# Kernel tuning notes

Measured on AMD Instinct MI355X. Metric: run time of the kernel, lower is better.

The kernel has to match this reference:

```python
import jax, jax.numpy as jnp
import numpy as np
from jax.scipy.special import i0

B, P = 2, 524288
N = (512, 512)            # uniform frequency grid
M = 4                     # window cutoff m (2M taps per dim)
SIGMA = 2.0
NGRID = tuple(2 * (int(SIGMA * Ni) // 2) for Ni in N)  # oversampled grid (1024, 1024)
BETA = tuple(float(np.pi * (2.0 - 1.0 / (ng / Ni))) for ng, Ni in zip(NGRID, N))


def _phi_hat_1d(Ni, ni, b):
    # Fourier coefficients of the Kaiser-Bessel window, k = -Ni/2 .. Ni/2-1
    k = jnp.arange(-Ni // 2, Ni // 2, dtype=jnp.float32)
    arg = jnp.sqrt(b * b - (2.0 * jnp.pi * k / ni) ** 2)
    return i0(M * arg) / ni


def _window_ft():
    # separable d-dim Fourier coefficient grid, shape [N1, N2] (== window.ft)
    c1 = _phi_hat_1d(N[0], NGRID[0], BETA[0])
    c2 = _phi_hat_1d(N[1], NGRID[1], BETA[1])
    return c1[:, None] * c2[None, :]


def _phi(t, ni, b):
    # Kaiser-Bessel window in time domain, support |t| <= M/ni
    u2 = M * M - (ni * t) ** 2
    u = jnp.sqrt(jnp.maximum(u2, 1e-12))
    return jnp.where(u2 > 0, jnp.sinh(b * u) / (jnp.pi * u), 0.0)


def setup_inputs() -> dict:
    key = jax.random.key(0)
    k1, k2 = jax.random.split(key)
    x = jax.random.uniform(k1, (B, P, 2), jnp.float32, -0.5, 0.5)  # points on torus
    f_hat = jax.random.normal(k2, (B, N[0], N[1], 2), jnp.float32)  # complex as [re,im]
    return {"x": x, "f_hat": f_hat}


def _nfft_forward(x, f_hat):
    # f(x_j) ~= sum_k f_hat[k] exp(-2 pi i <k, x_j>) via window-deconvolved oversampled FFT + local gather
    fh = (f_hat[..., 0] + 1j * f_hat[..., 1]).astype(jnp.complex64)  # [B, N1, N2]
    ft = _window_ft().astype(jnp.float32)
    gh = fh / ft                                                    # deconvolve
    p1 = (NGRID[0] - N[0]) // 2
    p2 = (NGRID[1] - N[1]) // 2
    gh = jnp.pad(gh, ((0, 0), (p1, p1), (p2, p2)))                  # centered zero-pad to n
    g = jnp.fft.fftn(jnp.fft.ifftshift(gh, axes=(-2, -1)), axes=(-2, -1))
    g = g / (NGRID[0] * NGRID[1])                                   # g_l = (1/n) sum_k gh_k e^{-2pi i kl/n}

    offs = jnp.arange(-M + 1, M + 1)                                # [2M]
    ws, idxs = [], []
    for d in range(2):
        nd = NGRID[d]
        xd = x[..., d]                                              # [B, P]
        l0 = jnp.floor(xd * nd).astype(jnp.int32)
        l = l0[..., None] + offs                                    # [B, P, 2M]
        t = xd[..., None] - l.astype(jnp.float32) / nd
        ws.append(_phi(t, nd, BETA[d]))
        idxs.append(jnp.mod(l, nd))

    g_flat = g.reshape(B, NGRID[0] * NGRID[1])
    acc = jnp.zeros((B, P), jnp.complex64)
    for i in range(2 * M):                                          # fixed 2m x 2m taps
        for j in range(2 * M):
            flat = idxs[0][..., i] * NGRID[1] + idxs[1][..., j]     # [B, P]
            gv = jnp.take_along_axis(g_flat, flat, axis=1)
            acc = acc + (ws[0][..., i] * ws[1][..., j]) * gv
    return jnp.stack([acc.real, acc.imag], axis=-1)                 # [B, P, 2]


def reference(x, f_hat):
    return _nfft_forward(x, f_hat)
```

## Files before the change

### kernel.cpp

```cpp
#include <hip/hip_runtime.h>

constexpr int   NGRID = 1024;
constexpr int   BATCH = 2;
constexpr int   NPTS  = 524288;
constexpr int   BINS  = 2048;
constexpr int   CAP   = 768;
constexpr float BETA  = 4.71238898038469f;
constexpr float PI_F  = 3.14159265358979f;

#define PIDX(i) ((i) + ((i) >> 4))

constexpr size_t G_BYTES  = (size_t)BATCH * NGRID * NGRID * sizeof(float2);
constexpr size_t GCNT_OFF = G_BYTES;
constexpr size_t PERM_OFF = G_BYTES + 8192;

__device__ __forceinline__ float i0f_large(float x) {
    float t = 3.75f / x;
    float p =  0.00392377f;
    p = p * t + -0.01647633f;
    p = p * t +  0.02635537f;
    p = p * t + -0.02057706f;
    p = p * t +  0.00916281f;
    p = p * t + -0.00157565f;
    p = p * t +  0.00225319f;
    p = p * t +  0.01328592f;
    p = p * t +  0.39894228f;
    return __expf(x) * rsqrtf(x) * p;
}

__device__ __forceinline__ int tile_of(float2 xv, int b) {
    int c1 = ((int)floorf(xv.x * 1024.0f)) & 1023;
    int c2 = ((int)floorf(xv.y * 1024.0f)) & 1023;
    return (b << 10) + ((c1 >> 5) << 5) + (c2 >> 5);
}

__device__ __forceinline__ float2 cmul(float2 a, float2 w) {
    return make_float2(a.x * w.x - a.y * w.y, a.x * w.y + a.y * w.x);
}

__device__ __forceinline__ int digitrev4_10(int f) {
    unsigned r = __brev((unsigned)f) >> 22;
    return (int)(((r & 0x2AAu) >> 1) | ((r & 0x155u) << 1));
}

__device__ __forceinline__ void build_tw4(float2* T, int tid, int nthreads) {
    int off = 0, q = 256, sig = 1;
    #pragma unroll
    for (int st = 0; st < 5; ++st) {
        for (int m = tid; m < 3 * q; m += nthreads) {
            int sec = 0, j = m;
            if (j >= q) { sec++; j -= q; }
            if (j >= q) { sec++; j -= q; }
            float ang = (-2.0f * PI_F / 1024.0f) * (float)((sec + 1) * j * sig);
            float sw, cw;
            __sincosf(ang, &sw, &cw);
            T[off + m] = make_float2(cw, sw);
        }
        off += 3 * q; q >>= 2; sig <<= 2;
    }
}

__device__ __forceinline__ void bfly4(float2* s, const float2* T,
                                      int bt, int q, int off) {
    int j    = bt & (q - 1);
    int base = ((bt - j) << 2) + j;
    int p0 = PIDX(base), p1 = PIDX(base + q);
    int p2 = PIDX(base + 2 * q), p3 = PIDX(base + 3 * q);
    float2 a0 = s[p0], a1 = s[p1], a2 = s[p2], a3 = s[p3];
    float2 t0 = make_float2(a0.x + a2.x, a0.y + a2.y);
    float2 t1 = make_float2(a0.x - a2.x, a0.y - a2.y);
    float2 t2 = make_float2(a1.x + a3.x, a1.y + a3.y);
    float2 t3 = make_float2(a1.x - a3.x, a1.y - a3.y);
    float2 b0 = make_float2(t0.x + t2.x, t0.y + t2.y);
    float2 b2 = make_float2(t0.x - t2.x, t0.y - t2.y);
    float2 b1 = make_float2(t1.x + t3.y, t1.y - t3.x);
    float2 b3 = make_float2(t1.x - t3.y, t1.y + t3.x);
    s[p0] = b0;
    s[p1] = cmul(b1, T[off + j]);
    s[p2] = cmul(b2, T[off + q + j]);
    s[p3] = cmul(b3, T[off + 2 * q + j]);
}

__global__ __launch_bounds__(256) void rows_and_bin(const float2* __restrict__ fh,
                                                    float2* __restrict__ g,
                                                    const float2* __restrict__ x,
                                                    int* __restrict__ gcnt,
                                                    float4* __restrict__ perm) {
    __shared__ __align__(16) char smem[16880];
    int tid = threadIdx.x;

    if (blockIdx.x < 1024) {
        float2* s = (float2*)smem;
        float2* T = (float2*)smem + 1087;
        int blk = blockIdx.x & 511;
        int b   = blockIdx.x >> 9;
        int row = (blk < 256) ? blk : blk + 512;
        int a1  = (row + 256) & 1023;

        build_tw4(T, tid, 256);

        float k1 = (float)(a1 - 256);
        float w1 = (2.0f * PI_F / 1024.0f) * k1;
        float c1 = i0f_large(4.0f * sqrtf(BETA * BETA - w1 * w1));

        const float2* fr = fh + ((long)b << 18) + ((long)a1 << 9);

        float w2a = (2.0f * PI_F / 1024.0f) * (float)tid;
        float c2a = i0f_large(4.0f * sqrtf(BETA * BETA - w2a * w2a));
        float w2b = (2.0f * PI_F / 1024.0f) * (float)(tid - 256);
        float c2b = i0f_large(4.0f * sqrtf(BETA * BETA - w2b * w2b));

        float2 va = fr[tid + 256];
        float2 vb = fr[tid];
        float ia = 1.0f / (c1 * c2a);
        float ib = 1.0f / (c1 * c2b);
        float2 A = make_float2(va.x * ia, va.y * ia);
        float2 B = make_float2(vb.x * ib, vb.y * ib);

        __syncthreads();

        s[PIDX(tid)]       = make_float2(A.x + B.x, A.y + B.y);
        s[PIDX(tid + 256)] = cmul(make_float2(A.x - B.y, A.y + B.x), T[tid]);
        s[PIDX(tid + 512)] = cmul(make_float2(A.x - B.x, A.y - B.y), T[256 + tid]);
        s[PIDX(tid + 768)] = cmul(make_float2(A.x + B.y, A.y - B.x), T[512 + tid]);

        int off = 768, q = 64;
        #pragma unroll
        for (int st = 0; st < 4; ++st) {
            __syncthreads();
            bfly4(s, T, tid, q, off);
            off += 3 * q; q >>= 2;
        }
        __syncthreads();

        float2* base = g + ((long)b << 20) + ((long)row << 10);
        #pragma unroll
        for (int i = 0; i < 4; ++i) {
            int idx = tid + (i << 8);
            base[idx] = s[PIDX(digitrev4_10(idx))];
        }
    } else {
        int* h = (int*)smem;
        int bblk = blockIdx.x - 1024;
        for (int i = tid; i < BINS; i += 256) h[i] = 0;
        __syncthreads();

        int base = bblk * 4096;
        int    tile[16];
        float2 pv[16];
        #pragma unroll
        for (int i = 0; i < 16; ++i) {
            int gid = base + tid + i * 256;
            pv[i]   = x[gid];
            tile[i] = tile_of(pv[i], gid >> 19);
            atomicAdd(&h[tile[i]], 1);
        }
        __syncthreads();

        #pragma unroll
        for (int j = 0; j < 8; ++j) {
            int bi = tid + j * 256;
            int c  = h[bi];
            h[bi]  = c ? atomicAdd(&gcnt[bi], c) : 0;
        }
        __syncthreads();

        #pragma unroll
        for (int i = 0; i < 16; ++i) {
            int gid = base + tid + i * 256;
            int pos = atomicAdd(&h[tile[i]], 1);
            perm[tile[i] * CAP + pos] =
                make_float4(pv[i].x, pv[i].y, __int_as_float(gid), 0.0f);
        }
    }
}

__global__ __launch_bounds__(256) void fft_cols(float2* __restrict__ g) {
    constexpr int STR = 1092;
    __shared__ float2 s[4 * STR];
    __shared__ float2 T[1023];
    int b  = blockIdx.y;
    int C0 = blockIdx.x * 4;
    int t  = threadIdx.x;
    int c  = t & 3, L = t >> 2;
    float2* gb = g + ((long)b << 20);

    build_tw4(T, t, 256);

    float2 E[16];
    #pragma unroll
    for (int m = 0; m < 4; ++m) {
        int r = L + 64 * m;
        E[m] = gb[((long)r << 10) + C0 + c];
    }
    #pragma unroll
    for (int m = 12; m < 16; ++m) {
        int r = L + 64 * m;
        E[m] = gb[((long)r << 10) + C0 + c];
    }
    __syncthreads();

    #pragma unroll
    for (int m = 0; m < 4; ++m) {
        float2 A = E[m], B = E[m + 12];
        int j = L + 64 * m;
        E[m]      = make_float2(A.x + B.x, A.y + B.y);
        E[m + 4]  = cmul(make_float2(A.x - B.y, A.y + B.x), T[j]);
        E[m + 8]  = cmul(make_float2(A.x - B.x, A.y - B.y), T[256 + j]);
        E[m + 12] = cmul(make_float2(A.x + B.y, A.y - B.x), T[512 + j]);
    }

    {
        float2 u1 = T[768 + L], u2 = T[768 + 64 + L], u3 = T[768 + 128 + L];
        #pragma unroll
        for (int a = 0; a < 4; ++a) {
            float2 a0 = E[4*a], a1 = E[4*a+1], a2 = E[4*a+2], a3 = E[4*a+3];
            float2 t0 = make_float2(a0.x + a2.x, a0.y + a2.y);
            float2 t1 = make_float2(a0.x - a2.x, a0.y - a2.y);
            float2 t2 = make_float2(a1.x + a3.x, a1.y + a3.y);
            float2 t3 = make_float2(a1.x - a3.x, a1.y - a3.y);
            E[4*a]   = make_float2(t0.x + t2.x, t0.y + t2.y);
            E[4*a+1] = cmul(make_float2(t1.x + t3.y, t1.y - t3.x), u1);
            E[4*a+2] = cmul(make_float2(t0.x - t2.x, t0.y - t2.y), u2);
            E[4*a+3] = cmul(make_float2(t1.x - t3.y, t1.y + t3.x), u3);
        }
    }

    float2* sf = s + c * STR;
    #pragma unroll
    for (int m = 0; m < 16; ++m) sf[PIDX(L + 64 * m)] = E[m];

    int off = 960, q = 16;
    #pragma unroll
    for (int st = 0; st < 3; ++st) {
        __syncthreads();
        #pragma unroll
        for (int rr = 0; rr < 4; ++rr)
            bfly4(sf, T, L + rr * 64, q, off);
        off += 3 * q; q >>= 2;
    }
    __syncthreads();

    #pragma unroll
    for (int i = 0; i < 16; ++i) {
        int r = L + i * 64;
        gb[((long)r << 10) + C0 + c] = sf[PIDX(digitrev4_10(r))];
    }
}

__global__ __launch_bounds__(256) void gather_binned(const float2* __restrict__ g,
                                                     const int* __restrict__ gcnt,
                                                     const float4* __restrict__ perm,
                                                     float2* __restrict__ out) {
    __shared__ float2 patch[37 * 37];
    int tb = blockIdx.x;
    int b  = tb >> 10;
    int tt = tb & 1023;
    int tR = tt >> 5, tC = tt & 31;
    int R0 = (tR << 5) - 2, C0 = (tC << 5) - 2;
    const float2* gb = g + ((long)b << 20);

    for (int p = threadIdx.x; p < 37 * 37; p += 256) {
        int pr = p / 37, pc = p - pr * 37;
        int gr = (R0 + pr) & 1023, gc = (C0 + pc) & 1023;
        patch[p] = gb[(gr << 10) + gc];
    }
    __syncthreads();

    int cnt = gcnt[tb];
    if (cnt > CAP) cnt = CAP;
    int off0 = tb * CAP;
    for (int i = (int)threadIdx.x; i < cnt; i += 256) {
        float4 rec = perm[off0 + i];
        int gid = __float_as_int(rec.z);

        float w1[6], w2[6];
        int rr0, cc0;
        {
            float xs = rec.x * 1024.0f;
            float fl = floorf(xs);
            float fr = xs - fl;
            rr0 = (((int)fl) & 1023) - (tR << 5);
            #pragma unroll
            for (int k = 0; k < 6; ++k) {
                float tv = fr - (float)(k - 2);
                float u2 = 16.0f - tv * tv;
                float ir = rsqrtf(u2);
                float z  = BETA * u2 * ir;
                w1[k] = __expf(z) * 0.159154943f * ir;
            }
        }
        {
            float xs = rec.y * 1024.0f;
            float fl = floorf(xs);
            float fr = xs - fl;
            cc0 = (((int)fl) & 1023) - (tC << 5);
            #pragma unroll
            for (int k = 0; k < 6; ++k) {
                float tv = fr - (float)(k - 2);
                float u2 = 16.0f - tv * tv;
                float ir = rsqrtf(u2);
                float z  = BETA * u2 * ir;
                w2[k] = __expf(z) * 0.159154943f * ir;
            }
        }

        float ar = 0.0f, ai = 0.0f;
        #pragma unroll
        for (int ii = 0; ii < 6; ++ii) {
            int pbase = (rr0 + ii) * 37 + cc0;
            float wi = w1[ii];
            #pragma unroll
            for (int jj = 0; jj < 6; ++jj) {
                float2 gv = patch[pbase + jj];
                float w = wi * w2[jj];
                ar = fmaf(w, gv.x, ar);
                ai = fmaf(w, gv.y, ai);
            }
        }
        out[gid] = make_float2(ar, ai);
    }
}

extern "C" void kernel_launch(void* const* d_in, const int* in_sizes, int n_in,
                              void* d_out, int out_size, void* d_ws, size_t ws_size,
                              hipStream_t stream) {
    const float2* x  = (const float2*)d_in[0];
    const float2* fh = (const float2*)d_in[1];
    char* ws = (char*)d_ws;
    float2* g    = (float2*)ws;
    int*    gcnt = (int*)(ws + GCNT_OFF);
    float4* perm = (float4*)(ws + PERM_OFF);

    hipMemsetAsync(gcnt, 0, BINS * sizeof(int), stream);

    rows_and_bin<<<dim3(1280), dim3(256), 0, stream>>>(fh, g, x, gcnt, perm);
    fft_cols    <<<dim3(256, BATCH), dim3(256), 0, stream>>>(g);

    gather_binned<<<dim3(BINS), dim3(256), 0, stream>>>(g, gcnt, perm, (float2*)d_out);
}
```

Measured before the change: 118.6 us.

## Fuse row FFT, binning, column FFT and gather into one persistent kernel

Replaces the three kernel launches with a single persistent kernel of 512 blocks. Each block processes several row-FFT, binning, column-FFT and gather work units, and software grid barriers built on atomic counters separate the phases. Twiddle tables are built once per block instead of once per launch, and launch gaps between phases go away. The cost is a spin-wait barrier that requires all 512 blocks to be co-resident, which risks deadlock if occupancy is too low. The gather phase also gets fewer blocks in flight, which may hurt latency hiding.

Result: slower. 266.9 us (+125.0%).

```diff
diff --git a/kernel.cpp b/kernel.cpp
--- a/kernel.cpp
+++ b/kernel.cpp
@@ -1,18 +1,22 @@
 #include <hip/hip_runtime.h>
 
-constexpr int   NGRID = 1024;
 constexpr int   BATCH = 2;
 constexpr int   NPTS  = 524288;
 constexpr int   BINS  = 2048;
 constexpr int   CAP   = 768;
+constexpr int   NBLK  = 512;
 constexpr float BETA  = 4.71238898038469f;
 constexpr float PI_F  = 3.14159265358979f;
 
 #define PIDX(i) ((i) + ((i) >> 4))
 
-constexpr size_t G_BYTES  = (size_t)BATCH * NGRID * NGRID * sizeof(float2);
+constexpr size_t G_BYTES  = (size_t)BATCH * 1024 * 1024 * sizeof(float2);
 constexpr size_t GCNT_OFF = G_BYTES;
-constexpr size_t PERM_OFF = G_BYTES + 8192;
+constexpr size_t BAR_OFF  = G_BYTES + 8192;
+constexpr size_t PERM_OFF = G_BYTES + 8192 + 64;
+
+constexpr int SMEM_BYTES = 43128;
+constexpr int T_F2_OFF   = 4368;
 
 __device__ __forceinline__ float i0f_large(float x) {
     float t = 3.75f / x;
@@ -81,111 +85,111 @@
     s[p3] = cmul(b3, T[off + 2 * q + j]);
 }
 
-__global__ __launch_bounds__(256) void rows_and_bin(const float2* __restrict__ fh,
-                                                    float2* __restrict__ g,
-                                                    const float2* __restrict__ x,
-                                                    int* __restrict__ gcnt,
-                                                    float4* __restrict__ perm) {
-    __shared__ __align__(16) char smem[16880];
-    int tid = threadIdx.x;
-
-    if (blockIdx.x < 1024) {
-        float2* s = (float2*)smem;
-        float2* T = (float2*)smem + 1087;
-        int blk = blockIdx.x & 511;
-        int b   = blockIdx.x >> 9;
-        int row = (blk < 256) ? blk : blk + 512;
-        int a1  = (row + 256) & 1023;
-
-        build_tw4(T, tid, 256);
-
-        float k1 = (float)(a1 - 256);
-        float w1 = (2.0f * PI_F / 1024.0f) * k1;
-        float c1 = i0f_large(4.0f * sqrtf(BETA * BETA - w1 * w1));
-
-        const float2* fr = fh + ((long)b << 18) + ((long)a1 << 9);
-
-        float w2a = (2.0f * PI_F / 1024.0f) * (float)tid;
-        float c2a = i0f_large(4.0f * sqrtf(BETA * BETA - w2a * w2a));
-        float w2b = (2.0f * PI_F / 1024.0f) * (float)(tid - 256);
-        float c2b = i0f_large(4.0f * sqrtf(BETA * BETA - w2b * w2b));
-
-        float2 va = fr[tid + 256];
-        float2 vb = fr[tid];
-        float ia = 1.0f / (c1 * c2a);
-        float ib = 1.0f / (c1 * c2b);
-        float2 A = make_float2(va.x * ia, va.y * ia);
-        float2 B = make_float2(vb.x * ib, vb.y * ib);
-
+__device__ __forceinline__ void grid_barrier(int* ctr) {
+    __syncthreads();
+    if (threadIdx.x == 0) {
+        __threadfence();
+        atomicAdd(ctr, 1);
+        while (atomicAdd(ctr, 0) < NBLK) __builtin_amdgcn_s_sleep(1);
+        __threadfence();
+    }
+    __syncthreads();
+}
+
+__device__ __forceinline__ void row_unit(int u, const float2* __restrict__ fh,
+                                         float2* __restrict__ g,
+                                         float2* s, const float2* T, int tid) {
+    int blk = u & 511;
+    int b   = u >> 9;
+    int row = (blk < 256) ? blk : blk + 512;
+    int a1  = (row + 256) & 1023;
+
+    float k1 = (float)(a1 - 256);
+    float w1 = (2.0f * PI_F / 1024.0f) * k1;
+    float c1 = i0f_large(4.0f * sqrtf(BETA * BETA - w1 * w1));
+
+    const float2* fr = fh + ((long)b << 18) + ((long)a1 << 9);
+
+    float w2a = (2.0f * PI_F / 1024.0f) * (float)tid;
+    float c2a = i0f_large(4.0f * sqrtf(BETA * BETA - w2a * w2a));
+    float w2b = (2.0f * PI_F / 1024.0f) * (float)(tid - 256);
+    float c2b = i0f_large(4.0f * sqrtf(BETA * BETA - w2b * w2b));
+
+    float2 va = fr[tid + 256];
+    float2 vb = fr[tid];
+    float ia = 1.0f / (c1 * c2a);
+    float ib = 1.0f / (c1 * c2b);
+    float2 A = make_float2(va.x * ia, va.y * ia);
+    float2 B = make_float2(vb.x * ib, vb.y * ib);
+
+    __syncthreads();
+
+    s[PIDX(tid)]       = make_float2(A.x + B.x, A.y + B.y);
+    s[PIDX(tid + 256)] = cmul(make_float2(A.x - B.y, A.y + B.x), T[tid]);
+    s[PIDX(tid + 512)] = cmul(make_float2(A.x - B.x, A.y - B.y), T[256 + tid]);
+    s[PIDX(tid + 768)] = cmul(make_float2(A.x + B.y, A.y - B.x), T[512 + tid]);
+
+    int off = 768, q = 64;
+    #pragma unroll
+    for (int st = 0; st < 4; ++st) {
         __syncthreads();
-
-        s[PIDX(tid)]       = make_float2(A.x + B.x, A.y + B.y);
-        s[PIDX(tid + 256)] = cmul(make_float2(A.x - B.y, A.y + B.x), T[tid]);
-        s[PIDX(tid + 512)] = cmul(make_float2(A.x - B.x, A.y - B.y), T[256 + tid]);
-        s[PIDX(tid + 768)] = cmul(make_float2(A.x + B.y, A.y - B.x), T[512 + tid]);
-
-        int off = 768, q = 64;
-        #pragma unroll
-        for (int st = 0; st < 4; ++st) {
-            __syncthreads();
-            bfly4(s, T, tid, q, off);
-            off += 3 * q; q >>= 2;
-        }
-        __syncthreads();
-
-        float2* base = g + ((long)b << 20) + ((long)row << 10);
-        #pragma unroll
-        for (int i = 0; i < 4; ++i) {
-            int idx = tid + (i << 8);
-            base[idx] = s[PIDX(digitrev4_10(idx))];
-        }
-    } else {
-        int* h = (int*)smem;
-        int bblk = blockIdx.x - 1024;
-        for (int i = tid; i < BINS; i += 256) h[i] = 0;
-        __syncthreads();
-
-        int base = bblk * 4096;
-        int    tile[16];
-        float2 pv[16];
-        #pragma unroll
-        for (int i = 0; i < 16; ++i) {
-            int gid = base + tid + i * 256;
-            pv[i]   = x[gid];
-            tile[i] = tile_of(pv[i], gid >> 19);
-            atomicAdd(&h[tile[i]], 1);
-        }
-        __syncthreads();
-
-        #pragma unroll
-        for (int j = 0; j < 8; ++j) {
-            int bi = tid + j * 256;
-            int c  = h[bi];
-            h[bi]  = c ? atomicAdd(&gcnt[bi], c) : 0;
-        }
-        __syncthreads();
-
-        #pragma unroll
-        for (int i = 0; i < 16; ++i) {
-            int gid = base + tid + i * 256;
-            int pos = atomicAdd(&h[tile[i]], 1);
-            perm[tile[i] * CAP + pos] =
-                make_float4(pv[i].x, pv[i].y, __int_as_float(gid), 0.0f);
-        }
-    }
-}
-
-__global__ __launch_bounds__(256) void fft_cols(float2* __restrict__ g) {
+        bfly4(s, T, tid, q, off);
+        off += 3 * q; q >>= 2;
+    }
+    __syncthreads();
+
+    float2* base = g + ((long)b << 20) + ((long)row << 10);
+    #pragma unroll
+    for (int i = 0; i < 4; ++i) {
+        int idx = tid + (i << 8);
+        base[idx] = s[PIDX(digitrev4_10(idx))];
+    }
+}
+
+__device__ __forceinline__ void bin_unit(int u, const float2* __restrict__ x,
+                                         int* __restrict__ gcnt,
+                                         float4* __restrict__ perm,
+                                         int* h, int tid) {
+    __syncthreads();
+    for (int i = tid; i < BINS; i += 256) h[i] = 0;
+    __syncthreads();
+
+    int base = u * 2048;
+    int    tile[8];
+    float2 pv[8];
+    #pragma unroll
+    for (int i = 0; i < 8; ++i) {
+        int gid = base + tid + i * 256;
+        pv[i]   = x[gid];
+        tile[i] = tile_of(pv[i], gid >> 19);
+        atomicAdd(&h[tile[i]], 1);
+    }
+    __syncthreads();
+
+    #pragma unroll
+    for (int j = 0; j < 8; ++j) {
+        int bi = tid + j * 256;
+        int c  = h[bi];
+        h[bi]  = c ? atomicAdd(&gcnt[bi], c) : 0;
+    }
+    __syncthreads();
+
+    #pragma unroll
+    for (int i = 0; i < 8; ++i) {
+        int gid = base + tid + i * 256;
+        int pos = atomicAdd(&h[tile[i]], 1);
+        perm[tile[i] * CAP + pos] =
+            make_float4(pv[i].x, pv[i].y, __int_as_float(gid), 0.0f);
+    }
+}
+
+__device__ __forceinline__ void cols_unit(int u, float2* __restrict__ g,
+                                          float2* s, const float2* T, int t) {
     constexpr int STR = 1092;
-    __shared__ float2 s[4 * STR];
-    __shared__ float2 T[1023];
-    int b  = blockIdx.y;
-    int C0 = blockIdx.x * 4;
-    int t  = threadIdx.x;
+    int b  = u >> 8;
+    int C0 = (u & 255) * 4;
     int c  = t & 3, L = t >> 2;
     float2* gb = g + ((long)b << 20);
-
-    build_tw4(T, t, 256);
 
     float2 E[16];
     #pragma unroll
@@ -198,7 +202,6 @@
         int r = L + 64 * m;
         E[m] = gb[((long)r << 10) + C0 + c];
     }
-    __syncthreads();
 
     #pragma unroll
     for (int m = 0; m < 4; ++m) {
@@ -248,19 +251,19 @@
     }
 }
 
-__global__ __launch_bounds__(256) void gather_binned(const float2* __restrict__ g,
-                                                     const int* __restrict__ gcnt,
-                                                     const float4* __restrict__ perm,
-                                                     float2* __restrict__ out) {
-    __shared__ float2 patch[37 * 37];
-    int tb = blockIdx.x;
+__device__ __forceinline__ void gather_unit(int tb, const float2* __restrict__ g,
+                                            const int* __restrict__ gcnt,
+                                            const float4* __restrict__ perm,
+                                            float2* __restrict__ out,
+                                            float2* patch, int tid) {
     int b  = tb >> 10;
     int tt = tb & 1023;
     int tR = tt >> 5, tC = tt & 31;
     int R0 = (tR << 5) - 2, C0 = (tC << 5) - 2;
     const float2* gb = g + ((long)b << 20);
 
-    for (int p = threadIdx.x; p < 37 * 37; p += 256) {
+    __syncthreads();
+    for (int p = tid; p < 37 * 37; p += 256) {
         int pr = p / 37, pc = p - pr * 37;
         int gr = (R0 + pr) & 1023, gc = (C0 + pc) & 1023;
         patch[p] = gb[(gr << 10) + gc];
@@ -270,7 +273,7 @@
     int cnt = gcnt[tb];
     if (cnt > CAP) cnt = CAP;
     int off0 = tb * CAP;
-    for (int i = (int)threadIdx.x; i < cnt; i += 256) {
+    for (int i = tid; i < cnt; i += 256) {
         float4 rec = perm[off0 + i];
         int gid = __float_as_int(rec.z);
 
@@ -322,6 +325,36 @@
     }
 }
 
+__global__ __launch_bounds__(256, 2) void mega(const float2* __restrict__ fh,
+                                               float2* __restrict__ g,
+                                               const float2* __restrict__ x,
+                                               int* __restrict__ gcnt,
+                                               float4* __restrict__ perm,
+                                               float2* __restrict__ out,
+                                               int* __restrict__ bar) {
+    __shared__ __align__(16) char smem[SMEM_BYTES];
+    float2* S = (float2*)smem;
+    float2* T = (float2*)smem + T_F2_OFF;
+    int tid = threadIdx.x, bid = blockIdx.x;
+
+    build_tw4(T, tid, 256);
+    __syncthreads();
+
+    row_unit(bid,        fh, g, S, T, tid);
+    row_unit(bid + NBLK, fh, g, S, T, tid);
+    bin_unit(bid, x, gcnt, perm, (int*)smem, tid);
+
+    grid_barrier(&bar[0]);
+
+    cols_unit(bid, g, S, T, tid);
+
+    grid_barrier(&bar[1]);
+
+    #pragma unroll
+    for (int i = 0; i < 4; ++i)
+        gather_unit(bid + i * NBLK, g, gcnt, perm, out, S, tid);
+}
+
 extern "C" void kernel_launch(void* const* d_in, const int* in_sizes, int n_in,
                               void* d_out, int out_size, void* d_ws, size_t ws_size,
                               hipStream_t stream) {
@@ -330,12 +363,10 @@
     char* ws = (char*)d_ws;
     float2* g    = (float2*)ws;
     int*    gcnt = (int*)(ws + GCNT_OFF);
+    int*    bar  = (int*)(ws + BAR_OFF);
     float4* perm = (float4*)(ws + PERM_OFF);
 
-    hipMemsetAsync(gcnt, 0, BINS * sizeof(int), stream);
-
-    rows_and_bin<<<dim3(1280), dim3(256), 0, stream>>>(fh, g, x, gcnt, perm);
-    fft_cols    <<<dim3(256, BATCH), dim3(256), 0, stream>>>(g);
-
-    gather_binned<<<dim3(BINS), dim3(256), 0, stream>>>(g, gcnt, perm, (float2*)d_out);
-}
+    hipMemsetAsync(gcnt, 0, 8192 + 64, stream);
+    mega<<<dim3(NBLK), dim3(256), 0, stream>>>(fh, g, x, gcnt, perm,
+                                               (float2*)d_out, bar);
+}
```
